# Kernel tuning notes

Hardware: AMD Instinct MI355X
Metric: run time of the kernel (lower is better)

Reference implementation:

```python
import jax, jax.numpy as jnp
import numpy as np

C_IN = 128
C_OUT = 128
P = 3
V = 4096
FIFO_SIZE = 17  # 2*kernel_size - 1, kernel_size = 9


def setup_inputs() -> dict:
    key = jax.random.key(0)
    k1, k2, k3, k4 = jax.random.split(key, 4)
    x = jax.random.normal(k1, (1, C_IN, V, 1), dtype=jnp.float32)
    A = jax.random.uniform(k2, (P, V, V), dtype=jnp.float32) / V  # roughly normalized adjacency
    fifo = jax.random.normal(k3, (FIFO_SIZE, P, C_OUT, V), dtype=jnp.float32)
    W = jax.random.normal(k4, (P * C_OUT, C_IN), dtype=jnp.float32) * 0.02  # 1x1 conv weight
    b = jnp.zeros((P * C_OUT,), dtype=jnp.float32)
    return {"x": x, "A": A, "fifo": fifo, "W": W, "b": b}


def reference(x, A, fifo, W, b):
    # x: (1, C_in, V, 1) single graph frame; residual = identity (C_in == C_out, stride 1)
    xv = x[0, :, :, 0]                                   # (C_in, V)
    # 1x1 conv -> split into P partitions: (P, C_out, V)
    z = (W @ xv + b[:, None]).reshape(P, C_OUT, V)
    # per-partition adjacency matmul: (P, C_out, V) @ (P, V, V)
    d = jnp.einsum('pcv,pvw->pcw', z, A)
    # FIFO push: newest frame in front, drop oldest
    new_fifo = jnp.concatenate([d[None], fifo[:FIFO_SIZE - 1]], axis=0)  # (FIFO, P, C_out, V)
    # temporal + partition reduction
    e = new_fifo.sum(axis=(0, 1))                        # (C_out, V)
    out = jax.nn.relu(e + xv)[None]                      # (1, C_out, V)
    return out
```

## Files before the change

kernel.cpp:

```cpp
#include <hip/hip_runtime.h>

typedef float f32x4 __attribute__((ext_vector_type(4)));
typedef __bf16 bf16x8 __attribute__((ext_vector_type(8)));
typedef unsigned short u16x4 __attribute__((ext_vector_type(4)));
typedef unsigned int u32x4 __attribute__((ext_vector_type(4)));

constexpr int V  = 4096;
constexpr int KS = 5;
constexpr int NSLAB = 3 * KS;

__device__ __forceinline__ unsigned short f2bf(float f) {
    unsigned int u = __float_as_uint(f);
    u += 0x7FFFu + ((u >> 16) & 1u);
    return (unsigned short)(u >> 16);
}
__device__ __forceinline__ float bf2f(unsigned short h) {
    return __uint_as_float(((unsigned int)h) << 16);
}

__global__ __launch_bounds__(256) void k_z(const float* __restrict__ x,
                                           const float* __restrict__ W,
                                           const float* __restrict__ b,
                                           unsigned short* __restrict__ zb) {
    __shared__ float Ws[8 * 128];
    __shared__ float bs[8];
    const int rg = blockIdx.x;
    const int vb = blockIdx.y;
    const int t  = threadIdx.x;
    reinterpret_cast<f32x4*>(Ws)[t] = reinterpret_cast<const f32x4*>(W + rg * 1024)[t];
    if (t < 8) bs[t] = b[rg * 8 + t];
    __syncthreads();
    const int v = vb * 1024 + t * 4;
    f32x4 acc[8] = {};
    #pragma unroll 8
    for (int j = 0; j < 128; ++j) {
        f32x4 xv = *reinterpret_cast<const f32x4*>(x + (size_t)j * V + v);
        #pragma unroll
        for (int q = 0; q < 8; ++q) acc[q] += Ws[q * 128 + j] * xv;
    }
    #pragma unroll
    for (int q = 0; q < 8; ++q) {
        u16x4 u;
        #pragma unroll
        for (int j = 0; j < 4; ++j) u[j] = f2bf(acc[q][j] + bs[q]);
        *reinterpret_cast<u16x4*>(zb + (size_t)(rg * 8 + q) * V + v) = u;
    }
}

__global__ __launch_bounds__(256, 2) void k_gemm(const unsigned short* __restrict__ zb,
                                                 const float* __restrict__ A,
                                                 unsigned short* __restrict__ partial) {
    __shared__ unsigned int Bt[2][256][20];

    const int nt = blockIdx.x;
    const int p  = blockIdx.y;
    const int kh = blockIdx.z;
    const int n0    = nt * 256;
    const int kbase = kh * 832;
    const int kend  = (kh == 4) ? 4096 : kbase + 832;

    const int t  = threadIdx.x;
    const int w  = t >> 6;
    const int l  = t & 63;
    const int wm = w >> 1, wn = w & 1;
    const int lrow = l & 15, g = l >> 4;

    const float* Ab = A + (size_t)p * V * V + (size_t)(w * 8) * V + n0 + l * 4;
    const int wswz = (w ^ (l & 3)) << 2;
    const int gp = (g ^ ((lrow >> 2) & 3)) << 2;
    const unsigned short* Zb = zb + ((size_t)p * 128 + wm * 64 + lrow) * V + g * 8;

    f32x4 acc[4][8] = {};
    f32x4 arA[8], arB[8];
    bf16x8 zr[4];

#define LOADA(AR, K) { _Pragma("unroll") for (int j = 0; j < 8; ++j) \
        AR[j] = *reinterpret_cast<const f32x4*>(Ab + (size_t)((K) + j) * V); }

#define LOADZ(K) { _Pragma("unroll") for (int mt = 0; mt < 4; ++mt) \
        zr[mt] = *reinterpret_cast<const bf16x8*>(Zb + (size_t)mt * 16 * V + (K)); }

#define WRITEB(B, AR) { _Pragma("unroll") for (int q = 0; q < 4; ++q) { \
        u32x4 pk; \
        asm("v_cvt_pk_bf16_f32 %0, %1, %2" : "=v"(pk[0]) : "v"(AR[0][q]), "v"(AR[1][q])); \
        asm("v_cvt_pk_bf16_f32 %0, %1, %2" : "=v"(pk[1]) : "v"(AR[2][q]), "v"(AR[3][q])); \
        asm("v_cvt_pk_bf16_f32 %0, %1, %2" : "=v"(pk[2]) : "v"(AR[4][q]), "v"(AR[5][q])); \
        asm("v_cvt_pk_bf16_f32 %0, %1, %2" : "=v"(pk[3]) : "v"(AR[6][q]), "v"(AR[7][q])); \
        *reinterpret_cast<u32x4*>(&Bt[B][l * 4 + q][wswz]) = pk; } }

#define BAR asm volatile("s_waitcnt lgkmcnt(0)\n\ts_barrier" ::: "memory")

#define MFMAP(B) { _Pragma("unroll") for (int nn = 0; nn < 8; ++nn) { \
        bf16x8 bf = *reinterpret_cast<const bf16x8*>(&Bt[B][wn * 128 + nn * 16 + lrow][gp]); \
        _Pragma("unroll") for (int mt = 0; mt < 4; ++mt) \
            acc[mt][nn] = __builtin_amdgcn_mfma_f32_16x16x32_bf16(zr[mt], bf, acc[mt][nn], 0, 0, 0); } }

    LOADA(arA, kbase);
    LOADZ(kbase);

    for (int k0 = kbase; k0 < kend; k0 += 64) {
        const int k1 = k0 + 32;
        const int k2 = (k0 + 64 < kend) ? k0 + 64 : kbase;
        WRITEB(0, arA);
        LOADA(arB, k1);
        BAR;
        MFMAP(0);
        LOADZ(k1);
        WRITEB(1, arB);
        LOADA(arA, k2);
        BAR;
        MFMAP(1);
        LOADZ(k2);
    }

    unsigned short* Pp = partial + (size_t)(p * KS + kh) * 128 * V;
    #pragma unroll
    for (int mt = 0; mt < 4; ++mt)
        #pragma unroll
        for (int nn = 0; nn < 8; ++nn) {
            const size_t base = (size_t)(wm * 64 + mt * 16 + g * 4) * V
                              + n0 + wn * 128 + nn * 16 + lrow;
            #pragma unroll
            for (int r = 0; r < 4; ++r)
                Pp[base + (size_t)r * V] = f2bf(acc[mt][nn][r]);
        }
#undef LOADA
#undef LOADZ
#undef WRITEB
#undef BAR
#undef MFMAP
}

__global__ __launch_bounds__(256) void k_epi(const float* __restrict__ x,
                                             const float* __restrict__ fifo,
                                             const unsigned short* __restrict__ partial,
                                             float* __restrict__ out) {
    const size_t off  = ((size_t)blockIdx.x * 256 + threadIdx.x) * 4;
    const size_t slab = (size_t)128 * V;
    f32x4 s0 = *reinterpret_cast<const f32x4*>(x + off);
    f32x4 s1 = {}, s2 = {}, s3 = {};
    #pragma unroll
    for (int s = 0; s < 48; ++s) {
        f32x4 fv = *reinterpret_cast<const f32x4*>(fifo + (size_t)s * slab + off);
        switch (s & 3) {
            case 0: s0 += fv; break;
            case 1: s1 += fv; break;
            case 2: s2 += fv; break;
            default: s3 += fv; break;
        }
    }
    #pragma unroll
    for (int q = 0; q < NSLAB; ++q) {
        u16x4 pv = *reinterpret_cast<const u16x4*>(partial + (size_t)q * slab + off);
        f32x4 d;
        #pragma unroll
        for (int j = 0; j < 4; ++j) d[j] = bf2f(pv[j]);
        if (q & 1) s1 += d; else s2 += d;
    }
    f32x4 sum = (s0 + s1) + (s2 + s3);
    f32x4 o;
    #pragma unroll
    for (int j = 0; j < 4; ++j) o[j] = fmaxf(sum[j], 0.0f);
    *reinterpret_cast<f32x4*>(out + off) = o;
}

extern "C" void kernel_launch(void* const* d_in, const int* in_sizes, int n_in,
                              void* d_out, int out_size, void* d_ws, size_t ws_size,
                              hipStream_t stream) {
    const float* x    = (const float*)d_in[0];
    const float* A    = (const float*)d_in[1];
    const float* fifo = (const float*)d_in[2];
    const float* W    = (const float*)d_in[3];
    const float* b    = (const float*)d_in[4];
    float* out = (float*)d_out;

    unsigned short* zb      = (unsigned short*)d_ws;
    unsigned short* partial = (unsigned short*)((char*)d_ws + (size_t)3 * 1024 * 1024);

    k_z   <<<dim3(48, 4),    256, 0, stream>>>(x, W, b, zb);
    k_gemm<<<dim3(16, 3, KS), 256, 0, stream>>>(zb, A, partial);
    k_epi <<<dim3(512),      256, 0, stream>>>(x, fifo, partial, out);
}
```

Baseline: 92.68 us.

## Overlap FIFO reduction with adjacency GEMM by interleaving blocks in one kernel

The 48-slab FIFO sum plus x moves out of the epilogue into 128 extra blocks that share a launch with the GEMM blocks, interleaved every third block id. The bandwidth-bound FIFO read can then run while the GEMM blocks work, and the final kernel only sums the pre-reduced fsum with the bf16 partials. The cost is an extra fp32 fsum buffer written and read back, and possible contention between the two block types on the same CUs.

```diff
diff --git a/kernel.cpp b/kernel.cpp
--- a/kernel.cpp
+++ b/kernel.cpp
@@ -47,19 +47,48 @@
     }
 }
 
-__global__ __launch_bounds__(256, 2) void k_gemm(const unsigned short* __restrict__ zb,
-                                                 const float* __restrict__ A,
-                                                 unsigned short* __restrict__ partial) {
+__global__ __launch_bounds__(256, 2) void k_fused(const unsigned short* __restrict__ zb,
+                                                  const float* __restrict__ A,
+                                                  const float* __restrict__ x,
+                                                  const float* __restrict__ fifo,
+                                                  unsigned short* __restrict__ partial,
+                                                  float* __restrict__ fsum) {
     __shared__ unsigned int Bt[2][256][20];
-
-    const int nt = blockIdx.x;
-    const int p  = blockIdx.y;
-    const int kh = blockIdx.z;
+    const int bid = blockIdx.x;
+    const int t   = threadIdx.x;
+
+    if (bid % 3 == 1) {
+        const int rid = bid / 3;
+        const size_t slab = (size_t)128 * V;
+        for (int i = 0; i < 4; ++i) {
+            const size_t off = ((size_t)(rid + 128 * i) * 256 + t) * 4;
+            f32x4 s0 = *reinterpret_cast<const f32x4*>(x + off);
+            f32x4 s1 = {}, s2 = {}, s3 = {};
+            #pragma unroll
+            for (int s = 0; s < 48; ++s) {
+                f32x4 fv = *reinterpret_cast<const f32x4*>(fifo + (size_t)s * slab + off);
+                switch (s & 3) {
+                    case 0: s0 += fv; break;
+                    case 1: s1 += fv; break;
+                    case 2: s2 += fv; break;
+                    default: s3 += fv; break;
+                }
+            }
+            *reinterpret_cast<f32x4*>(fsum + off) = (s0 + s1) + (s2 + s3);
+        }
+        return;
+    }
+
+    const int aid = bid - (bid + 1) / 3;
+    if (aid >= 240) return;
+    const int nt = aid & 15;
+    const int rest = aid >> 4;
+    const int p  = rest % 3;
+    const int kh = rest / 3;
     const int n0    = nt * 256;
     const int kbase = kh * 832;
     const int kend  = (kh == 4) ? 4096 : kbase + 832;
 
-    const int t  = threadIdx.x;
     const int w  = t >> 6;
     const int l  = t & 63;
     const int wm = w >> 1, wn = w & 1;
@@ -131,33 +160,22 @@
 #undef MFMAP
 }
 
-__global__ __launch_bounds__(256) void k_epi(const float* __restrict__ x,
-                                             const float* __restrict__ fifo,
-                                             const unsigned short* __restrict__ partial,
-                                             float* __restrict__ out) {
+__global__ __launch_bounds__(256) void k_epi2(const float* __restrict__ fsum,
+                                              const unsigned short* __restrict__ partial,
+                                              float* __restrict__ out) {
     const size_t off  = ((size_t)blockIdx.x * 256 + threadIdx.x) * 4;
     const size_t slab = (size_t)128 * V;
-    f32x4 s0 = *reinterpret_cast<const f32x4*>(x + off);
-    f32x4 s1 = {}, s2 = {}, s3 = {};
-    #pragma unroll
-    for (int s = 0; s < 48; ++s) {
-        f32x4 fv = *reinterpret_cast<const f32x4*>(fifo + (size_t)s * slab + off);
-        switch (s & 3) {
-            case 0: s0 += fv; break;
-            case 1: s1 += fv; break;
-            case 2: s2 += fv; break;
-            default: s3 += fv; break;
-        }
-    }
+    f32x4 s0 = *reinterpret_cast<const f32x4*>(fsum + off);
+    f32x4 s1 = {};
     #pragma unroll
     for (int q = 0; q < NSLAB; ++q) {
         u16x4 pv = *reinterpret_cast<const u16x4*>(partial + (size_t)q * slab + off);
         f32x4 d;
         #pragma unroll
         for (int j = 0; j < 4; ++j) d[j] = bf2f(pv[j]);
-        if (q & 1) s1 += d; else s2 += d;
-    }
-    f32x4 sum = (s0 + s1) + (s2 + s3);
+        if (q & 1) s1 += d; else s0 += d;
+    }
+    f32x4 sum = s0 + s1;
     f32x4 o;
     #pragma unroll
     for (int j = 0; j < 4; ++j) o[j] = fmaxf(sum[j], 0.0f);
@@ -176,8 +194,9 @@
 
     unsigned short* zb      = (unsigned short*)d_ws;
     unsigned short* partial = (unsigned short*)((char*)d_ws + (size_t)3 * 1024 * 1024);
-
-    k_z   <<<dim3(48, 4),    256, 0, stream>>>(x, W, b, zb);
-    k_gemm<<<dim3(16, 3, KS), 256, 0, stream>>>(zb, A, partial);
-    k_epi <<<dim3(512),      256, 0, stream>>>(x, fifo, partial, out);
-}
+    float*          fsum    = (float*)((char*)d_ws + (size_t)18 * 1024 * 1024);
+
+    k_z    <<<dim3(48, 4), 256, 0, stream>>>(x, W, b, zb);
+    k_fused<<<dim3(384),   256, 0, stream>>>(zb, A, x, fifo, partial, fsum);
+    k_epi2 <<<dim3(512),   256, 0, stream>>>(fsum, partial, out);
+}
```

After: 107.3 us. 1.16x slower.

## Fold FIFO reduction into GEMM kernel to overlap with A streaming

Applied to the files above, without the earlier changes.

The GEMM blocks now also load and sum most of the 48 FIFO slabs (plus x) for a 2048-element slice each, interleaved with the A-tile loads and MFMAs, and write a float partial sum. The epilogue reads that sum for the covered range and only reduces the FIFO directly for the remaining tail. This aims to hide the FIFO bandwidth cost behind the memory-bound GEMM instead of paying it in a separate pass, at the cost of more registers (launch bounds lowered to 1 block per CU) and extra memory traffic contending with the A stream.

```diff
diff --git a/kernel.cpp b/kernel.cpp
--- a/kernel.cpp
+++ b/kernel.cpp
@@ -8,6 +8,8 @@
 constexpr int V  = 4096;
 constexpr int KS = 5;
 constexpr int NSLAB = 3 * KS;
+constexpr size_t FSL = (size_t)128 * 4096;
+constexpr int FCOV = 240 * 2048;
 
 __device__ __forceinline__ unsigned short f2bf(float f) {
     unsigned int u = __float_as_uint(f);
@@ -47,9 +49,12 @@
     }
 }
 
-__global__ __launch_bounds__(256, 2) void k_gemm(const unsigned short* __restrict__ zb,
+__global__ __launch_bounds__(256, 1) void k_gemm(const unsigned short* __restrict__ zb,
                                                  const float* __restrict__ A,
-                                                 unsigned short* __restrict__ partial) {
+                                                 const float* __restrict__ x,
+                                                 const float* __restrict__ fifo,
+                                                 unsigned short* __restrict__ partial,
+                                                 float* __restrict__ fsum) {
     __shared__ unsigned int Bt[2][256][20];
 
     const int nt = blockIdx.x;
@@ -70,6 +75,13 @@
     const int gp = (g ^ ((lrow >> 2) & 3)) << 2;
     const unsigned short* Zb = zb + ((size_t)p * 128 + wm * 64 + lrow) * V + g * 8;
 
+    const int fbid = nt + 16 * (p + 3 * kh);
+    const size_t fo0 = (size_t)fbid * 2048 + t * 4;
+    const size_t fo1 = fo0 + 1024;
+    f32x4 facc0 = {}, facc1 = {};
+    f32x4 fA0, fA1, fA2, fA3, fB0, fB1, fB2, fB3;
+    int fs_issue = 2, fs_done = 0;
+
     f32x4 acc[4][8] = {};
     f32x4 arA[8], arB[8];
     bf16x8 zr[4];
@@ -79,6 +91,16 @@
 
 #define LOADZ(K) { _Pragma("unroll") for (int mt = 0; mt < 4; ++mt) \
         zr[mt] = *reinterpret_cast<const bf16x8*>(Zb + (size_t)mt * 16 * V + (K)); }
+
+#define LOADF(F0, F1, F2, F3) { if (fs_issue < 48) { \
+        F0 = *reinterpret_cast<const f32x4*>(fifo + (size_t)fs_issue * FSL + fo0); \
+        F1 = *reinterpret_cast<const f32x4*>(fifo + (size_t)fs_issue * FSL + fo1); \
+        F2 = *reinterpret_cast<const f32x4*>(fifo + (size_t)(fs_issue + 1) * FSL + fo0); \
+        F3 = *reinterpret_cast<const f32x4*>(fifo + (size_t)(fs_issue + 1) * FSL + fo1); \
+        fs_issue += 2; } }
+
+#define ACCF(F0, F1, F2, F3) { if (fs_done < 48) { \
+        facc0 += F0; facc1 += F1; facc0 += F2; facc1 += F3; fs_done += 2; } }
 
 #define WRITEB(B, AR) { _Pragma("unroll") for (int q = 0; q < 4; ++q) { \
         u32x4 pk; \
@@ -97,20 +119,28 @@
 
     LOADA(arA, kbase);
     LOADZ(kbase);
+    fA0 = *reinterpret_cast<const f32x4*>(fifo + fo0);
+    fA1 = *reinterpret_cast<const f32x4*>(fifo + fo1);
+    fA2 = *reinterpret_cast<const f32x4*>(fifo + FSL + fo0);
+    fA3 = *reinterpret_cast<const f32x4*>(fifo + FSL + fo1);
 
     for (int k0 = kbase; k0 < kend; k0 += 64) {
         const int k1 = k0 + 32;
-        const int k2 = (k0 + 64 < kend) ? k0 + 64 : kbase;
+        const bool pf = (k0 + 64) < kend;
         WRITEB(0, arA);
         LOADA(arB, k1);
+        LOADF(fB0, fB1, fB2, fB3);
         BAR;
         MFMAP(0);
+        ACCF(fA0, fA1, fA2, fA3);
         LOADZ(k1);
         WRITEB(1, arB);
-        LOADA(arA, k2);
+        if (pf) LOADA(arA, k0 + 64);
+        LOADF(fA0, fA1, fA2, fA3);
         BAR;
         MFMAP(1);
-        LOADZ(k2);
+        ACCF(fB0, fB1, fB2, fB3);
+        if (pf) LOADZ(k0 + 64);
     }
 
     unsigned short* Pp = partial + (size_t)(p * KS + kh) * 128 * V;
@@ -124,40 +154,46 @@
             for (int r = 0; r < 4; ++r)
                 Pp[base + (size_t)r * V] = f2bf(acc[mt][nn][r]);
         }
+
+    facc0 += *reinterpret_cast<const f32x4*>(x + fo0);
+    facc1 += *reinterpret_cast<const f32x4*>(x + fo1);
+    *reinterpret_cast<f32x4*>(fsum + fo0) = facc0;
+    *reinterpret_cast<f32x4*>(fsum + fo1) = facc1;
 #undef LOADA
 #undef LOADZ
+#undef LOADF
+#undef ACCF
 #undef WRITEB
 #undef BAR
 #undef MFMAP
 }
 
-__global__ __launch_bounds__(256) void k_epi(const float* __restrict__ x,
-                                             const float* __restrict__ fifo,
-                                             const unsigned short* __restrict__ partial,
-                                             float* __restrict__ out) {
-    const size_t off  = ((size_t)blockIdx.x * 256 + threadIdx.x) * 4;
-    const size_t slab = (size_t)128 * V;
-    f32x4 s0 = *reinterpret_cast<const f32x4*>(x + off);
-    f32x4 s1 = {}, s2 = {}, s3 = {};
-    #pragma unroll
-    for (int s = 0; s < 48; ++s) {
-        f32x4 fv = *reinterpret_cast<const f32x4*>(fifo + (size_t)s * slab + off);
-        switch (s & 3) {
-            case 0: s0 += fv; break;
-            case 1: s1 += fv; break;
-            case 2: s2 += fv; break;
-            default: s3 += fv; break;
+__global__ __launch_bounds__(256) void k_epi2(const float* __restrict__ x,
+                                              const float* __restrict__ fifo,
+                                              const float* __restrict__ fsum,
+                                              const unsigned short* __restrict__ partial,
+                                              float* __restrict__ out) {
+    const size_t off = ((size_t)blockIdx.x * 256 + threadIdx.x) * 4;
+    f32x4 s0, s1 = {};
+    if (off < (size_t)FCOV) {
+        s0 = *reinterpret_cast<const f32x4*>(fsum + off);
+    } else {
+        s0 = *reinterpret_cast<const f32x4*>(x + off);
+        #pragma unroll
+        for (int s = 0; s < 48; ++s) {
+            f32x4 fv = *reinterpret_cast<const f32x4*>(fifo + (size_t)s * FSL + off);
+            if (s & 1) s1 += fv; else s0 += fv;
         }
     }
     #pragma unroll
     for (int q = 0; q < NSLAB; ++q) {
-        u16x4 pv = *reinterpret_cast<const u16x4*>(partial + (size_t)q * slab + off);
+        u16x4 pv = *reinterpret_cast<const u16x4*>(partial + (size_t)q * FSL + off);
         f32x4 d;
         #pragma unroll
         for (int j = 0; j < 4; ++j) d[j] = bf2f(pv[j]);
-        if (q & 1) s1 += d; else s2 += d;
-    }
-    f32x4 sum = (s0 + s1) + (s2 + s3);
+        if (q & 1) s1 += d; else s0 += d;
+    }
+    f32x4 sum = s0 + s1;
     f32x4 o;
     #pragma unroll
     for (int j = 0; j < 4; ++j) o[j] = fmaxf(sum[j], 0.0f);
@@ -176,8 +212,9 @@
 
     unsigned short* zb      = (unsigned short*)d_ws;
     unsigned short* partial = (unsigned short*)((char*)d_ws + (size_t)3 * 1024 * 1024);
-
-    k_z   <<<dim3(48, 4),    256, 0, stream>>>(x, W, b, zb);
-    k_gemm<<<dim3(16, 3, KS), 256, 0, stream>>>(zb, A, partial);
-    k_epi <<<dim3(512),      256, 0, stream>>>(x, fifo, partial, out);
-}
+    float*          fsum    = (float*)((char*)d_ws + (size_t)18 * 1024 * 1024);
+
+    k_z   <<<dim3(48, 4),     256, 0, stream>>>(x, W, b, zb);
+    k_gemm<<<dim3(16, 3, KS), 256, 0, stream>>>(zb, A, x, fifo, partial, fsum);
+    k_epi2<<<dim3(512),       256, 0, stream>>>(x, fifo, fsum, partial, out);
+}
```

Measured after the change: 95.40 us. 1.03x slower.

## Widen GEMM tile to 512 columns with 512-thread blocks and finer K split

Applied to the files above, without the earlier changes.

The adjacency GEMM now uses 512-thread blocks covering 512 output columns. Each wave stages 4 rows of A over two 256-column halves, with a new LDS swizzle. The K dimension is split into 10 uneven slabs instead of 5, which keeps the grid at 240 blocks, and the wrap-around prefetch on the last iteration is replaced by a conditional skip. The intent is better reuse of the z operand per block and less redundant loading. In exchange the epilogue must read twice as many bf16 partial slabs, adding more partial write and read traffic.

```diff
diff --git a/kernel.cpp b/kernel.cpp
--- a/kernel.cpp
+++ b/kernel.cpp
@@ -3,10 +3,10 @@
 typedef float f32x4 __attribute__((ext_vector_type(4)));
 typedef __bf16 bf16x8 __attribute__((ext_vector_type(8)));
 typedef unsigned short u16x4 __attribute__((ext_vector_type(4)));
-typedef unsigned int u32x4 __attribute__((ext_vector_type(4)));
+typedef unsigned int u32x2 __attribute__((ext_vector_type(2)));
 
 constexpr int V  = 4096;
-constexpr int KS = 5;
+constexpr int KS = 10;
 constexpr int NSLAB = 3 * KS;
 
 __device__ __forceinline__ unsigned short f2bf(float f) {
@@ -47,51 +47,54 @@
     }
 }
 
-__global__ __launch_bounds__(256, 2) void k_gemm(const unsigned short* __restrict__ zb,
+__global__ __launch_bounds__(512, 1) void k_gemm(const unsigned short* __restrict__ zb,
                                                  const float* __restrict__ A,
                                                  unsigned short* __restrict__ partial) {
-    __shared__ unsigned int Bt[2][256][20];
+    __shared__ unsigned int Bt[2][512][20];
 
     const int nt = blockIdx.x;
     const int p  = blockIdx.y;
     const int kh = blockIdx.z;
-    const int n0    = nt * 256;
-    const int kbase = kh * 832;
-    const int kend  = (kh == 4) ? 4096 : kbase + 832;
+    const int n0    = nt * 512;
+    const int kbase = (kh < 6) ? kh * 384 : 2304 + (kh - 6) * 448;
+    const int kend  = kbase + ((kh < 6) ? 384 : 448);
 
     const int t  = threadIdx.x;
     const int w  = t >> 6;
     const int l  = t & 63;
-    const int wm = w >> 1, wn = w & 1;
+    const int wm = w >> 2;
+    const int wn = w & 3;
     const int lrow = l & 15, g = l >> 4;
 
-    const float* Ab = A + (size_t)p * V * V + (size_t)(w * 8) * V + n0 + l * 4;
-    const int wswz = (w ^ (l & 3)) << 2;
-    const int gp = (g ^ ((lrow >> 2) & 3)) << 2;
+    const float* Ab = A + (size_t)p * V * V + (size_t)(w * 4) * V + n0 + l * 4;
     const unsigned short* Zb = zb + ((size_t)p * 128 + wm * 64 + lrow) * V + g * 8;
+    const int wsl = (l >> 1) & 6;
 
     f32x4 acc[4][8] = {};
-    f32x4 arA[8], arB[8];
+    f32x4 arA[4][2], arB[4][2];
     bf16x8 zr[4];
 
-#define LOADA(AR, K) { _Pragma("unroll") for (int j = 0; j < 8; ++j) \
-        AR[j] = *reinterpret_cast<const f32x4*>(Ab + (size_t)((K) + j) * V); }
+#define LOADA(AR, K) { _Pragma("unroll") for (int j = 0; j < 4; ++j) { \
+        AR[j][0] = *reinterpret_cast<const f32x4*>(Ab + (size_t)((K) + j) * V); \
+        AR[j][1] = *reinterpret_cast<const f32x4*>(Ab + (size_t)((K) + j) * V + 256); } }
 
 #define LOADZ(K) { _Pragma("unroll") for (int mt = 0; mt < 4; ++mt) \
         zr[mt] = *reinterpret_cast<const bf16x8*>(Zb + (size_t)mt * 16 * V + (K)); }
 
-#define WRITEB(B, AR) { _Pragma("unroll") for (int q = 0; q < 4; ++q) { \
-        u32x4 pk; \
-        asm("v_cvt_pk_bf16_f32 %0, %1, %2" : "=v"(pk[0]) : "v"(AR[0][q]), "v"(AR[1][q])); \
-        asm("v_cvt_pk_bf16_f32 %0, %1, %2" : "=v"(pk[1]) : "v"(AR[2][q]), "v"(AR[3][q])); \
-        asm("v_cvt_pk_bf16_f32 %0, %1, %2" : "=v"(pk[2]) : "v"(AR[4][q]), "v"(AR[5][q])); \
-        asm("v_cvt_pk_bf16_f32 %0, %1, %2" : "=v"(pk[3]) : "v"(AR[6][q]), "v"(AR[7][q])); \
-        *reinterpret_cast<u32x4*>(&Bt[B][l * 4 + q][wswz]) = pk; } }
+#define WRITEB(B, AR) { const int s_ = 2 * (w ^ wsl); \
+        _Pragma("unroll") for (int h = 0; h < 2; ++h) \
+        _Pragma("unroll") for (int q = 0; q < 4; ++q) { \
+            u32x2 pk; \
+            asm("v_cvt_pk_bf16_f32 %0, %1, %2" : "=v"(pk[0]) : "v"(AR[0][h][q]), "v"(AR[1][h][q])); \
+            asm("v_cvt_pk_bf16_f32 %0, %1, %2" : "=v"(pk[1]) : "v"(AR[2][h][q]), "v"(AR[3][h][q])); \
+            *reinterpret_cast<u32x2*>(&Bt[B][h * 256 + l * 4 + q][s_]) = pk; } }
 
 #define BAR asm volatile("s_waitcnt lgkmcnt(0)\n\ts_barrier" ::: "memory")
 
 #define MFMAP(B) { _Pragma("unroll") for (int nn = 0; nn < 8; ++nn) { \
-        bf16x8 bf = *reinterpret_cast<const bf16x8*>(&Bt[B][wn * 128 + nn * 16 + lrow][gp]); \
+        const int n_ = wn * 128 + nn * 16 + lrow; \
+        const int s0_ = (2 * g) ^ ((n_ >> 3) & 6); \
+        bf16x8 bf = *reinterpret_cast<const bf16x8*>(&Bt[B][n_][2 * s0_]); \
         _Pragma("unroll") for (int mt = 0; mt < 4; ++mt) \
             acc[mt][nn] = __builtin_amdgcn_mfma_f32_16x16x32_bf16(zr[mt], bf, acc[mt][nn], 0, 0, 0); } }
 
@@ -99,18 +102,17 @@
     LOADZ(kbase);
 
     for (int k0 = kbase; k0 < kend; k0 += 64) {
-        const int k1 = k0 + 32;
-        const int k2 = (k0 + 64 < kend) ? k0 + 64 : kbase;
+        const bool pf = (k0 + 64) < kend;
         WRITEB(0, arA);
-        LOADA(arB, k1);
+        LOADA(arB, k0 + 32);
         BAR;
         MFMAP(0);
-        LOADZ(k1);
+        LOADZ(k0 + 32);
         WRITEB(1, arB);
-        LOADA(arA, k2);
+        if (pf) LOADA(arA, k0 + 64);
         BAR;
         MFMAP(1);
-        LOADZ(k2);
+        if (pf) LOADZ(k0 + 64);
     }
 
     unsigned short* Pp = partial + (size_t)(p * KS + kh) * 128 * V;
@@ -178,6 +180,6 @@
     unsigned short* partial = (unsigned short*)((char*)d_ws + (size_t)3 * 1024 * 1024);
 
     k_z   <<<dim3(48, 4),    256, 0, stream>>>(x, W, b, zb);
-    k_gemm<<<dim3(16, 3, KS), 256, 0, stream>>>(zb, A, partial);
+    k_gemm<<<dim3(8, 3, KS), 512, 0, stream>>>(zb, A, partial);
     k_epi <<<dim3(512),      256, 0, stream>>>(x, fifo, partial, out);
 }
```

Result: slower. 101.1 us (+9.0%).
